# Performance work log

Measured on AMD Instinct MI355X. Metric: run time of the kernel, lower is better.

## Reference

```python
import jax, jax.numpy as jnp
import numpy as np

N = 100000       # nodes
E = 1600000      # edges
NFEAT = 256
NHID = 128
NCLASS = 1


def setup_inputs() -> dict:
    key = jax.random.key(0)
    ks = jax.random.split(key, 9)
    x = jax.random.normal(ks[0], (N, NFEAT), dtype=jnp.float32)
    src = jax.random.randint(ks[1], (E,), 0, N, dtype=jnp.int32)
    dst = jax.random.randint(ks[2], (E,), 0, N, dtype=jnp.int32)
    W1 = jax.random.normal(ks[3], (NFEAT, NHID), dtype=jnp.float32) * (1.0 / np.sqrt(NFEAT))
    b1 = jnp.zeros((NHID,), dtype=jnp.float32)
    W2 = jax.random.normal(ks[4], (NHID, NHID), dtype=jnp.float32) * (1.0 / np.sqrt(NHID))
    b2 = jnp.zeros((NHID,), dtype=jnp.float32)
    Wfc = jax.random.normal(ks[5], (NHID, NCLASS), dtype=jnp.float32) * (1.0 / np.sqrt(NHID))
    bfc = jnp.zeros((NCLASS,), dtype=jnp.float32)
    return {"x": x, "W1": W1, "b1": b1, "W2": W2, "b2": b2,
            "Wfc": Wfc, "bfc": bfc, "src": src, "dst": dst}


def reference(x, W1, b1, W2, b2, Wfc, bfc, src, dst):
    # Symmetric GCN normalization (DGL GraphConv, norm='both').
    ones = jnp.ones((E,), dtype=jnp.float32)
    out_deg = jax.ops.segment_sum(ones, src, num_segments=N)
    in_deg = jax.ops.segment_sum(ones, dst, num_segments=N)
    norm_s = jnp.maximum(out_deg, 1.0) ** -0.5  # [N] src-side norm
    norm_d = jnp.maximum(in_deg, 1.0) ** -0.5   # [N] dst-side norm

    def gconv(h, W, b):
        # weight-before-aggregate (math-equivalent; minimizes [E, d] gather width)
        m = (h * norm_s[:, None]) @ W          # [N, out]
        agg = jax.ops.segment_sum(m[src], dst, num_segments=N)  # SpMM via gather+scatter-add
        return agg * norm_d[:, None] + b

    h1 = jax.nn.relu(gconv(x, W1, b1))
    # dropout is identity in eval mode
    h2 = gconv(h1, W2, b2)
    return h2 @ Wfc + bfc  # [N, NCLASS]
```

## Files before the change

### kernel.cpp

```cpp
#include <hip/hip_runtime.h>
#include <hip/hip_bf16.h>

#define NNODES 100000
#define NEDGES 1600000
#define NF 256
#define NH 128
#define SCAN_ELEMS 1024
#define SCAN_NBLK ((NNODES + SCAN_ELEMS - 1) / SCAN_ELEMS)

#define HG 200
#define HCHUNK (NEDGES / HG)
#define HBINS 50000
#define HR 2
#define HWORDS (NNODES / 2)

#define WPREP_BLOCKS 129

typedef _Float16 half4v __attribute__((ext_vector_type(4)));
typedef _Float16 half8v __attribute__((ext_vector_type(8)));
typedef float floatx16 __attribute__((ext_vector_type(16)));

__device__ __forceinline__ int pos16(int k) {
    return (((k >> 2) & 1) << 3) + (k & 3) + (((k >> 3) & 1) << 2);
}
__device__ __forceinline__ int ipos16(int p) {
    int g = (p >> 3) & 1, j = p & 7;
    return g * 4 + (j & 3) + ((j >> 2) << 3);
}

__device__ __forceinline__ float2 h2f2(unsigned u) {
    union { unsigned u; _Float16 h[2]; } c; c.u = u;
    return make_float2((float)c.h[0], (float)c.h[1]);
}

__device__ __forceinline__ void load_lds16(const void* g, void* l) {
    __builtin_amdgcn_global_load_lds(
        (const __attribute__((address_space(1))) void*)g,
        (__attribute__((address_space(3))) void*)l, 16, 0, 0);
}

__global__ __launch_bounds__(512)
void hist_part_kernel(const int* __restrict__ src, const int* __restrict__ dst,
                      unsigned* __restrict__ partial) {
    __shared__ unsigned lds[HBINS / 2];
    const int g = blockIdx.x, t = threadIdx.x;
    const int e0 = g * HCHUNK;
    for (int r = 0; r < HR; ++r) {
        const int lo = r * HBINS;
        for (int i = t; i < HBINS / 2; i += 512) lds[i] = 0;
        __syncthreads();
        for (int i = t; i < HCHUNK; i += 512) {
            unsigned us = (unsigned)(src[e0 + i] - lo);
            if (us < HBINS) atomicAdd(&lds[us >> 1], 1u << ((us & 1) * 16));
            unsigned ud = (unsigned)(dst[e0 + i] - lo);
            if (ud < HBINS) atomicAdd(&lds[ud >> 1], 1u << ((ud & 1) * 16 + 8));
        }
        __syncthreads();
        unsigned* dp = partial + (size_t)g * HWORDS + (lo >> 1);
        for (int i = t; i < HBINS / 2; i += 512) dp[i] = lds[i];
        __syncthreads();
    }
}

__global__ __launch_bounds__(256)
void degscan_kernel(const unsigned* __restrict__ partial,
                    unsigned char* __restrict__ offb,
                    float* __restrict__ ns, float* __restrict__ nd,
                    int* __restrict__ cnt_in) {
    int w = blockIdx.x * 256 + threadIdx.x;
    if (w >= HWORDS) return;
    unsigned o0 = 0, i0 = 0, o1 = 0, i1 = 0;
    for (int g0 = 0; g0 < HG; g0 += 8) {
        unsigned v[8];
        #pragma unroll
        for (int j = 0; j < 8; ++j) v[j] = partial[(size_t)(g0 + j) * HWORDS + w];
        #pragma unroll
        for (int j = 0; j < 8; ++j) {
            *(unsigned short*)(offb + (size_t)(g0 + j) * NNODES + 2 * w) =
                (unsigned short)((i0 & 0xffu) | ((i1 & 0xffu) << 8));
            o0 += v[j] & 0xffu;         i0 += (v[j] >> 8) & 0xffu;
            o1 += (v[j] >> 16) & 0xffu; i1 += v[j] >> 24;
        }
    }
    int n0 = 2 * w, n1 = 2 * w + 1;
    ns[n0] = rsqrtf((float)max((int)o0, 1));
    nd[n0] = rsqrtf((float)max((int)i0, 1));
    cnt_in[n0] = (int)i0;
    ns[n1] = rsqrtf((float)max((int)o1, 1));
    nd[n1] = rsqrtf((float)max((int)i1, 1));
    cnt_in[n1] = (int)i1;
}

__global__ __launch_bounds__(256)
void scanA_kernel(const int* __restrict__ cnt, int* __restrict__ pre,
                  int* __restrict__ bsum, int n) {
    __shared__ int tsum[256];
    int b = blockIdx.x, t = threadIdx.x;
    int base = b * SCAN_ELEMS + t * 4;
    int v[4]; int s = 0;
    #pragma unroll
    for (int k = 0; k < 4; ++k) { int idx = base + k; v[k] = (idx < n) ? cnt[idx] : 0; s += v[k]; }
    tsum[t] = s;
    __syncthreads();
    for (int off = 1; off < 256; off <<= 1) {
        int val = (t >= off) ? tsum[t - off] : 0;
        __syncthreads();
        tsum[t] += val;
        __syncthreads();
    }
    int run = (t == 0) ? 0 : tsum[t - 1];
    #pragma unroll
    for (int k = 0; k < 4; ++k) { int idx = base + k; if (idx < n) pre[idx] = run; run += v[k]; }
    if (t == 255) bsum[b] = tsum[255];
}

__global__ __launch_bounds__(128)
void scanB_kernel(int* __restrict__ bsum, int nb, int* __restrict__ row_ptr) {
    __shared__ int s[128];
    int t = threadIdx.x;
    int v = (t < nb) ? bsum[t] : 0;
    s[t] = v;
    __syncthreads();
    for (int off = 1; off < 128; off <<= 1) {
        int u = (t >= off) ? s[t - off] : 0;
        __syncthreads();
        s[t] += u;
        __syncthreads();
    }
    if (t < nb) bsum[t] = s[t] - v;
    if (t == 0) row_ptr[NNODES] = NEDGES;
}

__global__ __launch_bounds__(256)
void scanC_kernel(int* __restrict__ pre, const int* __restrict__ bsum, int n) {
    int add = bsum[blockIdx.x];
    int base = blockIdx.x * SCAN_ELEMS + threadIdx.x;
    #pragma unroll
    for (int k = 0; k < 4; ++k) {
        int idx = base + k * 256;
        if (idx < n) pre[idx] += add;
    }
}

__global__ __launch_bounds__(512)
void fill_kernel(const int* __restrict__ src, const int* __restrict__ dst,
                 const int* __restrict__ row_ptr, const unsigned char* __restrict__ offb,
                 int* __restrict__ col) {
    __shared__ unsigned lcur[HBINS / 2];
    const int g = blockIdx.x, t = threadIdx.x;
    const int e0 = g * HCHUNK;
    const unsigned char* ob = offb + (size_t)g * NNODES;
    for (int r = 0; r < HR; ++r) {
        const int lo = r * HBINS;
        for (int i = t; i < HBINS / 2; i += 512) lcur[i] = 0;
        __syncthreads();
        for (int i = t; i < HCHUNK; i += 512) {
            int d = dst[e0 + i];
            unsigned ud = (unsigned)(d - lo);
            if (ud < HBINS) {
                unsigned prev = atomicAdd(&lcur[ud >> 1], 1u << ((ud & 1) * 16));
                unsigned rank = (prev >> ((ud & 1) * 16)) & 0xffffu;
                int p = row_ptr[d] + (int)ob[d] + (int)rank;
                col[p] = src[e0 + i];
            }
        }
        __syncthreads();
    }
}

__global__ __launch_bounds__(256)
void prep_w_kernel(const float* __restrict__ W1, const float* __restrict__ b1,
                   _Float16* __restrict__ Wt1, float* __restrict__ b1p,
                   const float* __restrict__ W2, const float* __restrict__ Wfc,
                   const float* __restrict__ b2, const float* __restrict__ bfc,
                   float* __restrict__ v2p, float* __restrict__ c0) {
    int b = blockIdx.x, t = threadIdx.x;
    if (b < WPREP_BLOCKS) {
        int id = b * 256 + t;
        if (id < NF * NH) {
            int k = id >> 7, n = id & 127;
            Wt1[(size_t)n * NF + (k & ~15) + pos16(k & 15)] = (_Float16)W1[id];
        } else if (id < NF * NH + NH) {
            int pos = id - NF * NH;
            int k = (pos & ~15) + ipos16(pos & 15);
            b1p[pos] = b1[k];
        }
    } else {
        if (t < 128) {
            float s = 0.f;
            #pragma unroll 16
            for (int j = 0; j < 128; ++j) s += W2[t * 128 + j] * Wfc[j];
            v2p[(t & ~15) + pos16(t & 15)] = s;
        } else if (t < 192) {
            int lane = t - 128;
            float c = b2[lane] * Wfc[lane] + b2[lane + 64] * Wfc[lane + 64];
            #pragma unroll
            for (int off = 32; off > 0; off >>= 1) c += __shfl_down(c, off);
            if (lane == 0) c0[0] = c + bfc[0];
        }
    }
}

__global__ __launch_bounds__(256, 4)
void gemm1_kernel(const float* __restrict__ X, const _Float16* __restrict__ Wt,
                  const float* __restrict__ norm_s, _Float16* __restrict__ Cout,
                  int N) {
    __shared__ __align__(16) float As[2][128 * 32];
    const int tid = threadIdx.x;
    const int l = tid & 63, w = tid >> 6;
    const int wr = w >> 1, wc = w & 1;
    const int row0 = blockIdx.x * 128;

    const _Float16* Bb = Wt + (size_t)(wc * 64 + (l & 31)) * NF + (l >> 5) * 8;
    const int ar = wr * 64 + (l & 31);
    const int swz = ar & 7;
    const int g = l >> 5;
    const int lr = l >> 3, lc = l & 7;
    floatx16 acc[2][2] = {};

    #pragma unroll
    for (int i = 0; i < 4; ++i) {
        int R = w * 32 + i * 8;
        int r = R + lr;
        int grow = min(row0 + r, N - 1);
        int srcc = lc ^ (r & 7);
        load_lds16(X + (size_t)grow * NF + srcc * 4, &As[0][R * 32]);
    }

    for (int t = 0; t < 8; ++t) {
        const int cur = t & 1;
        if (t < 7) {
            #pragma unroll
            for (int i = 0; i < 4; ++i) {
                int R = w * 32 + i * 8;
                int r = R + lr;
                int grow = min(row0 + r, N - 1);
                int srcc = lc ^ (r & 7);
                load_lds16(X + (size_t)grow * NF + (t + 1) * 32 + srcc * 4,
                           &As[cur ^ 1][R * 32]);
            }
            __builtin_amdgcn_sched_barrier(0);
            asm volatile("s_waitcnt vmcnt(4)" ::: "memory");
            __builtin_amdgcn_sched_barrier(0);
        } else {
            __builtin_amdgcn_sched_barrier(0);
            asm volatile("s_waitcnt vmcnt(0)" ::: "memory");
            __builtin_amdgcn_sched_barrier(0);
        }
        __builtin_amdgcn_s_barrier();
        #pragma unroll
        for (int kk = 0; kk < 2; ++kk) {
            int ca = kk * 4 + g;
            int cb = ca + 2;
            float4 a0l = *(const float4*)&As[cur][(size_t)ar * 32 + (ca ^ swz) * 4];
            float4 a0h = *(const float4*)&As[cur][(size_t)ar * 32 + (cb ^ swz) * 4];
            float4 a1l = *(const float4*)&As[cur][(size_t)(ar + 32) * 32 + (ca ^ swz) * 4];
            float4 a1h = *(const float4*)&As[cur][(size_t)(ar + 32) * 32 + (cb ^ swz) * 4];
            half8v a0 = { (_Float16)a0l.x, (_Float16)a0l.y, (_Float16)a0l.z, (_Float16)a0l.w,
                          (_Float16)a0h.x, (_Float16)a0h.y, (_Float16)a0h.z, (_Float16)a0h.w };
            half8v a1 = { (_Float16)a1l.x, (_Float16)a1l.y, (_Float16)a1l.z, (_Float16)a1l.w,
                          (_Float16)a1h.x, (_Float16)a1h.y, (_Float16)a1h.z, (_Float16)a1h.w };
            const _Float16* bp = Bb + (t * 2 + kk) * 16;
            half8v b0 = *(const half8v*)bp;
            half8v b1 = *(const half8v*)(bp + (size_t)32 * NF);
            acc[0][0] = __builtin_amdgcn_mfma_f32_32x32x16_f16(a0, b0, acc[0][0], 0, 0, 0);
            acc[0][1] = __builtin_amdgcn_mfma_f32_32x32x16_f16(a0, b1, acc[0][1], 0, 0, 0);
            acc[1][0] = __builtin_amdgcn_mfma_f32_32x32x16_f16(a1, b0, acc[1][0], 0, 0, 0);
            acc[1][1] = __builtin_amdgcn_mfma_f32_32x32x16_f16(a1, b1, acc[1][1], 0, 0, 0);
        }
        __builtin_amdgcn_s_barrier();
    }

    const int cpos = pos16(l & 15);
    const int chi = ((l >> 4) & 1) << 4;
    #pragma unroll
    for (int m = 0; m < 2; ++m) {
        #pragma unroll
        for (int r = 0; r < 16; ++r) {
            int rloc = wr * 64 + m * 32 + (r & 3) + ((r >> 2) << 3) + ((l >> 5) << 2);
            int grow = row0 + rloc;
            if (grow < N) {
                float s = norm_s[grow];
                #pragma unroll
                for (int n = 0; n < 2; ++n) {
                    int colbase = wc * 64 + n * 32 + chi;
                    Cout[(size_t)grow * NH + colbase + cpos] = (_Float16)(acc[m][n][r] * s);
                }
            }
        }
    }
}

__global__ __launch_bounds__(512)
void gatherz_kernel(const _Float16* __restrict__ m, const int* __restrict__ row_ptr,
                    const int* __restrict__ col, const float* __restrict__ norm_d,
                    const float* __restrict__ norm_s, const float* __restrict__ b1p,
                    const float* __restrict__ v2p, float* __restrict__ z, int N) {
    int w = (blockIdx.x * 512 + threadIdx.x) >> 6;
    int lane = threadIdx.x & 63;
    if (w >= N) return;
    int beg = __builtin_amdgcn_readfirstlane(row_ptr[w]);
    int end = __builtin_amdgcn_readfirstlane(row_ptr[w + 1]);
    const unsigned* mu = (const unsigned*)m + lane;
    float ax = 0.f, ay = 0.f;
    int i = beg;
    for (; i + 15 < end; i += 16) {
        unsigned u[16];
        #pragma unroll
        for (int j = 0; j < 16; ++j) u[j] = mu[(size_t)col[i + j] * 64];
        #pragma unroll
        for (int j = 0; j < 16; ++j) { float2 v = h2f2(u[j]); ax += v.x; ay += v.y; }
    }
    for (; i + 3 < end; i += 4) {
        unsigned u[4];
        #pragma unroll
        for (int j = 0; j < 4; ++j) u[j] = mu[(size_t)col[i + j] * 64];
        #pragma unroll
        for (int j = 0; j < 4; ++j) { float2 v = h2f2(u[j]); ax += v.x; ay += v.y; }
    }
    for (; i < end; ++i) {
        float2 v = h2f2(mu[(size_t)col[i] * 64]);
        ax += v.x; ay += v.y;
    }
    float nd = norm_d[w], ns = norm_s[w];
    float2 bv = ((const float2*)b1p)[lane];
    float hx = fmaxf(fmaf(ax, nd, bv.x), 0.f) * ns;
    float hy = fmaxf(fmaf(ay, nd, bv.y), 0.f) * ns;
    float2 w2 = ((const float2*)v2p)[lane];
    float p = fmaf(hx, w2.x, hy * w2.y);
    #pragma unroll
    for (int off = 32; off > 0; off >>= 1) p += __shfl_down(p, off);
    if (lane == 0) z[w] = p;
}

__global__ __launch_bounds__(256)
void outsum_kernel(const float* __restrict__ z, const int* __restrict__ row_ptr,
                   const int* __restrict__ col, const float* __restrict__ norm_d,
                   const float* __restrict__ c0, float* __restrict__ out, int N) {
    int w = blockIdx.x * 256 + threadIdx.x;
    if (w >= N) return;
    int beg = row_ptr[w], end = row_ptr[w + 1];
    float s0 = 0.f, s1 = 0.f, s2 = 0.f, s3 = 0.f;
    int i = beg;
    for (; i + 3 < end; i += 4) {
        s0 += z[col[i]];     s1 += z[col[i + 1]];
        s2 += z[col[i + 2]]; s3 += z[col[i + 3]];
    }
    for (; i < end; ++i) s0 += z[col[i]];
    out[w] = norm_d[w] * ((s0 + s1) + (s2 + s3)) + c0[0];
}

extern "C" void kernel_launch(void* const* d_in, const int* in_sizes, int n_in,
                              void* d_out, int out_size, void* d_ws, size_t ws_size,
                              hipStream_t stream) {
    const float* x   = (const float*)d_in[0];
    const float* W1  = (const float*)d_in[1];
    const float* b1  = (const float*)d_in[2];
    const float* W2  = (const float*)d_in[3];
    const float* b2  = (const float*)d_in[4];
    const float* Wfc = (const float*)d_in[5];
    const float* bfc = (const float*)d_in[6];
    const int*   src = (const int*)d_in[7];
    const int*   dst = (const int*)d_in[8];
    float* out = (float*)d_out;

    const int N = NNODES, E = NEDGES;

    char* p = (char*)d_ws;
    float*    norm_s = (float*)p;      p += (size_t)N * 4;
    float*    norm_d = (float*)p;      p += (size_t)N * 4;
    _Float16* bufA_h = (_Float16*)p;   p += (size_t)N * NH * 2;
    _Float16* Wt1    = (_Float16*)p;   p += (size_t)NF * NH * 2;
    float*    b1p    = (float*)p;      p += NH * 4;
    float*    v2p    = (float*)p;      p += NH * 4;
    float*    c0     = (float*)p;      p += 16;
    float*    z      = (float*)p;      p += (size_t)N * 4;
    int*      cnt_in = (int*)p;        p += (size_t)N * 4;
    int*      row_ptr= (int*)p;        p += (size_t)(N + 1) * 4 + 12;
    int*      col    = (int*)p;        p += (size_t)E * 4;
    int*      bsum   = (int*)p;        p += 128 * 4;
    unsigned* partial= (unsigned*)p;
    unsigned char* offb = (unsigned char*)bufA_h;

    hist_part_kernel<<<HG, 512, 0, stream>>>(src, dst, partial);
    degscan_kernel<<<(HWORDS + 255) / 256, 256, 0, stream>>>(partial, offb, norm_s, norm_d, cnt_in);
    scanA_kernel<<<SCAN_NBLK, 256, 0, stream>>>(cnt_in, row_ptr, bsum, N);
    scanB_kernel<<<1, 128, 0, stream>>>(bsum, SCAN_NBLK, row_ptr);
    scanC_kernel<<<SCAN_NBLK, 256, 0, stream>>>(row_ptr, bsum, N);
    fill_kernel<<<HG, 512, 0, stream>>>(src, dst, row_ptr, offb, col);
    prep_w_kernel<<<WPREP_BLOCKS + 1, 256, 0, stream>>>(W1, b1, Wt1, b1p,
                                                        W2, Wfc, b2, bfc, v2p, c0);

    gemm1_kernel<<<(N + 127) / 128, 256, 0, stream>>>(x, Wt1, norm_s, bufA_h, N);
    gatherz_kernel<<<((size_t)N * 64 + 511) / 512, 512, 0, stream>>>(
        bufA_h, row_ptr, col, norm_d, norm_s, b1p, v2p, z, N);
    outsum_kernel<<<(N + 255) / 256, 256, 0, stream>>>(z, row_ptr, col, norm_d, c0, out, N);
}
```

Baseline: 197.3 us.

## Record per-edge ranks in histogram pass and split GEMM rows per wavefront

The histogram kernel now stores each edge's local rank within its chunk for its destination node (8-bit). That lets the CSR fill step run as a flat one-thread-per-edge kernel with no LDS atomics or repeated passes, in place of 200 blocks that redid the atomic counting. The GEMM kernel is also restructured so each wavefront owns 32 rows and all 128 output columns, with private LDS buffers and no block barriers. This adds 1.6 MB of rank writes and reads. It also assumes per-chunk in-degree counts fit in 8 bits and moves more B-operand global loads onto each wave.

```diff
diff --git a/kernel.cpp b/kernel.cpp
--- a/kernel.cpp
+++ b/kernel.cpp
@@ -41,7 +41,7 @@
 
 __global__ __launch_bounds__(512)
 void hist_part_kernel(const int* __restrict__ src, const int* __restrict__ dst,
-                      unsigned* __restrict__ partial) {
+                      unsigned* __restrict__ partial, unsigned char* __restrict__ rank8) {
     __shared__ unsigned lds[HBINS / 2];
     const int g = blockIdx.x, t = threadIdx.x;
     const int e0 = g * HCHUNK;
@@ -53,7 +53,11 @@
             unsigned us = (unsigned)(src[e0 + i] - lo);
             if (us < HBINS) atomicAdd(&lds[us >> 1], 1u << ((us & 1) * 16));
             unsigned ud = (unsigned)(dst[e0 + i] - lo);
-            if (ud < HBINS) atomicAdd(&lds[ud >> 1], 1u << ((ud & 1) * 16 + 8));
+            if (ud < HBINS) {
+                unsigned sh = (ud & 1) * 16 + 8;
+                unsigned prev = atomicAdd(&lds[ud >> 1], 1u << sh);
+                rank8[e0 + i] = (unsigned char)((prev >> sh) & 0xffu);
+            }
         }
         __syncthreads();
         unsigned* dp = partial + (size_t)g * HWORDS + (lo >> 1);
@@ -142,30 +146,17 @@
     }
 }
 
-__global__ __launch_bounds__(512)
+__global__ __launch_bounds__(256)
 void fill_kernel(const int* __restrict__ src, const int* __restrict__ dst,
+                 const unsigned char* __restrict__ rank8,
                  const int* __restrict__ row_ptr, const unsigned char* __restrict__ offb,
-                 int* __restrict__ col) {
-    __shared__ unsigned lcur[HBINS / 2];
-    const int g = blockIdx.x, t = threadIdx.x;
-    const int e0 = g * HCHUNK;
-    const unsigned char* ob = offb + (size_t)g * NNODES;
-    for (int r = 0; r < HR; ++r) {
-        const int lo = r * HBINS;
-        for (int i = t; i < HBINS / 2; i += 512) lcur[i] = 0;
-        __syncthreads();
-        for (int i = t; i < HCHUNK; i += 512) {
-            int d = dst[e0 + i];
-            unsigned ud = (unsigned)(d - lo);
-            if (ud < HBINS) {
-                unsigned prev = atomicAdd(&lcur[ud >> 1], 1u << ((ud & 1) * 16));
-                unsigned rank = (prev >> ((ud & 1) * 16)) & 0xffffu;
-                int p = row_ptr[d] + (int)ob[d] + (int)rank;
-                col[p] = src[e0 + i];
-            }
-        }
-        __syncthreads();
-    }
+                 int* __restrict__ col, int E) {
+    int e = blockIdx.x * 256 + threadIdx.x;
+    if (e >= E) return;
+    int d = dst[e];
+    int g = e / HCHUNK;
+    int pos = row_ptr[d] + (int)offb[(size_t)g * NNODES + d] + (int)rank8[e];
+    col[pos] = src[e];
 }
 
 __global__ __launch_bounds__(256)
@@ -205,39 +196,38 @@
 void gemm1_kernel(const float* __restrict__ X, const _Float16* __restrict__ Wt,
                   const float* __restrict__ norm_s, _Float16* __restrict__ Cout,
                   int N) {
-    __shared__ __align__(16) float As[2][128 * 32];
+    __shared__ __align__(16) float As[4][2][32 * 32];
     const int tid = threadIdx.x;
     const int l = tid & 63, w = tid >> 6;
-    const int wr = w >> 1, wc = w & 1;
-    const int row0 = blockIdx.x * 128;
-
-    const _Float16* Bb = Wt + (size_t)(wc * 64 + (l & 31)) * NF + (l >> 5) * 8;
-    const int ar = wr * 64 + (l & 31);
+    const int row0 = (blockIdx.x * 4 + w) * 32;
+    if (row0 >= N) return;
+
+    const int ar = l & 31;
     const int swz = ar & 7;
     const int g = l >> 5;
     const int lr = l >> 3, lc = l & 7;
-    floatx16 acc[2][2] = {};
+    float* buf0 = &As[w][0][0];
+    float* buf1 = &As[w][1][0];
+    floatx16 acc[4] = {};
 
     #pragma unroll
     for (int i = 0; i < 4; ++i) {
-        int R = w * 32 + i * 8;
-        int r = R + lr;
+        int r = i * 8 + lr;
         int grow = min(row0 + r, N - 1);
         int srcc = lc ^ (r & 7);
-        load_lds16(X + (size_t)grow * NF + srcc * 4, &As[0][R * 32]);
+        load_lds16(X + (size_t)grow * NF + srcc * 4, buf0 + i * 256);
     }
 
     for (int t = 0; t < 8; ++t) {
-        const int cur = t & 1;
+        float* cur = (t & 1) ? buf1 : buf0;
+        float* nxt = (t & 1) ? buf0 : buf1;
         if (t < 7) {
             #pragma unroll
             for (int i = 0; i < 4; ++i) {
-                int R = w * 32 + i * 8;
-                int r = R + lr;
+                int r = i * 8 + lr;
                 int grow = min(row0 + r, N - 1);
                 int srcc = lc ^ (r & 7);
-                load_lds16(X + (size_t)grow * NF + (t + 1) * 32 + srcc * 4,
-                           &As[cur ^ 1][R * 32]);
+                load_lds16(X + (size_t)grow * NF + (t + 1) * 32 + srcc * 4, nxt + i * 256);
             }
             __builtin_amdgcn_sched_barrier(0);
             asm volatile("s_waitcnt vmcnt(4)" ::: "memory");
@@ -247,46 +237,35 @@
             asm volatile("s_waitcnt vmcnt(0)" ::: "memory");
             __builtin_amdgcn_sched_barrier(0);
         }
-        __builtin_amdgcn_s_barrier();
         #pragma unroll
         for (int kk = 0; kk < 2; ++kk) {
             int ca = kk * 4 + g;
             int cb = ca + 2;
-            float4 a0l = *(const float4*)&As[cur][(size_t)ar * 32 + (ca ^ swz) * 4];
-            float4 a0h = *(const float4*)&As[cur][(size_t)ar * 32 + (cb ^ swz) * 4];
-            float4 a1l = *(const float4*)&As[cur][(size_t)(ar + 32) * 32 + (ca ^ swz) * 4];
-            float4 a1h = *(const float4*)&As[cur][(size_t)(ar + 32) * 32 + (cb ^ swz) * 4];
-            half8v a0 = { (_Float16)a0l.x, (_Float16)a0l.y, (_Float16)a0l.z, (_Float16)a0l.w,
-                          (_Float16)a0h.x, (_Float16)a0h.y, (_Float16)a0h.z, (_Float16)a0h.w };
-            half8v a1 = { (_Float16)a1l.x, (_Float16)a1l.y, (_Float16)a1l.z, (_Float16)a1l.w,
-                          (_Float16)a1h.x, (_Float16)a1h.y, (_Float16)a1h.z, (_Float16)a1h.w };
-            const _Float16* bp = Bb + (t * 2 + kk) * 16;
-            half8v b0 = *(const half8v*)bp;
-            half8v b1 = *(const half8v*)(bp + (size_t)32 * NF);
-            acc[0][0] = __builtin_amdgcn_mfma_f32_32x32x16_f16(a0, b0, acc[0][0], 0, 0, 0);
-            acc[0][1] = __builtin_amdgcn_mfma_f32_32x32x16_f16(a0, b1, acc[0][1], 0, 0, 0);
-            acc[1][0] = __builtin_amdgcn_mfma_f32_32x32x16_f16(a1, b0, acc[1][0], 0, 0, 0);
-            acc[1][1] = __builtin_amdgcn_mfma_f32_32x32x16_f16(a1, b1, acc[1][1], 0, 0, 0);
-        }
-        __builtin_amdgcn_s_barrier();
+            float4 al = *(const float4*)(cur + ar * 32 + (ca ^ swz) * 4);
+            float4 ah = *(const float4*)(cur + ar * 32 + (cb ^ swz) * 4);
+            half8v a0 = { (_Float16)al.x, (_Float16)al.y, (_Float16)al.z, (_Float16)al.w,
+                          (_Float16)ah.x, (_Float16)ah.y, (_Float16)ah.z, (_Float16)ah.w };
+            const _Float16* bp = Wt + (size_t)ar * NF + g * 8 + (t * 2 + kk) * 16;
+            #pragma unroll
+            for (int n = 0; n < 4; ++n) {
+                half8v b = *(const half8v*)(bp + (size_t)n * 32 * NF);
+                acc[n] = __builtin_amdgcn_mfma_f32_32x32x16_f16(a0, b, acc[n], 0, 0, 0);
+            }
+        }
     }
 
     const int cpos = pos16(l & 15);
     const int chi = ((l >> 4) & 1) << 4;
     #pragma unroll
-    for (int m = 0; m < 2; ++m) {
-        #pragma unroll
-        for (int r = 0; r < 16; ++r) {
-            int rloc = wr * 64 + m * 32 + (r & 3) + ((r >> 2) << 3) + ((l >> 5) << 2);
-            int grow = row0 + rloc;
-            if (grow < N) {
-                float s = norm_s[grow];
-                #pragma unroll
-                for (int n = 0; n < 2; ++n) {
-                    int colbase = wc * 64 + n * 32 + chi;
-                    Cout[(size_t)grow * NH + colbase + cpos] = (_Float16)(acc[m][n][r] * s);
-                }
-            }
+    for (int r = 0; r < 16; ++r) {
+        int rloc = (r & 3) + ((r >> 2) << 3) + ((l >> 5) << 2);
+        int grow = row0 + rloc;
+        if (grow < N) {
+            float s = norm_s[grow];
+            _Float16* crow = Cout + (size_t)grow * NH + chi + cpos;
+            #pragma unroll
+            for (int n = 0; n < 4; ++n)
+                crow[n * 32] = (_Float16)(acc[n][r] * s);
         }
     }
 }
@@ -379,15 +358,16 @@
     int*      row_ptr= (int*)p;        p += (size_t)(N + 1) * 4 + 12;
     int*      col    = (int*)p;        p += (size_t)E * 4;
     int*      bsum   = (int*)p;        p += 128 * 4;
+    unsigned char* rank8 = (unsigned char*)p;  p += (size_t)E;
     unsigned* partial= (unsigned*)p;
     unsigned char* offb = (unsigned char*)bufA_h;
 
-    hist_part_kernel<<<HG, 512, 0, stream>>>(src, dst, partial);
+    hist_part_kernel<<<HG, 512, 0, stream>>>(src, dst, partial, rank8);
     degscan_kernel<<<(HWORDS + 255) / 256, 256, 0, stream>>>(partial, offb, norm_s, norm_d, cnt_in);
     scanA_kernel<<<SCAN_NBLK, 256, 0, stream>>>(cnt_in, row_ptr, bsum, N);
     scanB_kernel<<<1, 128, 0, stream>>>(bsum, SCAN_NBLK, row_ptr);
     scanC_kernel<<<SCAN_NBLK, 256, 0, stream>>>(row_ptr, bsum, N);
-    fill_kernel<<<HG, 512, 0, stream>>>(src, dst, row_ptr, offb, col);
+    fill_kernel<<<(E + 255) / 256, 256, 0, stream>>>(src, dst, rank8, row_ptr, offb, col, E);
     prep_w_kernel<<<WPREP_BLOCKS + 1, 256, 0, stream>>>(W1, b1, Wt1, b1p,
                                                         W2, Wfc, b2, bfc, v2p, c0);
 
```

New measurement: 210.0 us. +6.5%, slower.
